# Optimization experiments

Hardware: AMD Instinct MI355X
Metric: run time of the kernel (lower is better)

Reference implementation:

```python
import jax, jax.numpy as jnp
import numpy as np

MARGIN = 0.2


def setup_inputs() -> dict:
    key = jax.random.key(0)
    k1, k2 = jax.random.split(key)
    N, D = 8192, 256
    im = jax.random.normal(k1, (N, D), dtype=jnp.float32)
    s = jax.random.normal(k2, (N, D), dtype=jnp.float32)
    return {"im": im, "s": s}


def reference(im, s):
    # scores[i, j] = <im_i, s_j>  (raw dot product, as in cosine_sim's mm)
    scores = im @ s.T                      # [N, N]
    diag = jnp.diagonal(scores)            # [N]

    # Rank of the diagonal element within each row / column of an ascending
    # sort == number of elements strictly smaller than it. This replaces the
    # original sort + host-side index search; weight = 1 / (rank + 1).
    # Ranks come from comparisons, so they carry no gradient (matching the
    # detached numpy computation in the original).
    rank1 = jnp.sum(scores < diag[:, None], axis=1)   # row rank of diag
    rank2 = jnp.sum(scores < diag[None, :], axis=0)   # col rank of diag
    w1 = 1.0 / (rank1.astype(scores.dtype) + 1.0)
    w2 = 1.0 / (rank2.astype(scores.dtype) + 1.0)

    # Hinge costs against the matched (diagonal) score.
    cost_s = jnp.maximum(MARGIN + scores - diag[:, None], 0.0)   # caption-retrieval
    cost_im = jnp.maximum(MARGIN + scores - diag[None, :], 0.0)  # image-retrieval

    # Zero out the diagonal (positive pairs).
    off_diag = ~jnp.eye(scores.shape[0], dtype=bool)
    cost_s = jnp.where(off_diag, cost_s, 0.0)
    cost_im = jnp.where(off_diag, cost_im, 0.0)

    # Hardest negative per row / column, rank-weighted.
    cost_s = w1 * jnp.max(cost_s, axis=1)
    cost_im = w2 * jnp.max(cost_im, axis=0)
    return jnp.sum(cost_s) + jnp.sum(cost_im)
```

## Files before the change

### kernel.cpp

```cpp
#include <hip/hip_runtime.h>
#include <stdint.h>

#define NROWS 8192
#define DDIM  256
#define K2    512
#define BLKSTRIDE 131072
#define MARGIN_F 0.2f
#define MFMA16 __builtin_amdgcn_mfma_f32_16x16x32_bf16
#define SBAR0() __builtin_amdgcn_sched_barrier(0)

typedef short  short8  __attribute__((ext_vector_type(8)));
typedef float  floatx4 __attribute__((ext_vector_type(4)));

__device__ unsigned short gA[(size_t)NROWS * K2];
__device__ unsigned short gB[(size_t)NROWS * K2];
__device__ float    g_diag[NROWS];
__device__ unsigned g_rowcnt[NROWS];
__device__ unsigned g_rowkey[NROWS];
__device__ unsigned g_colcnt[NROWS];
__device__ unsigned g_colkey[NROWS];

__device__ __forceinline__ unsigned short f2bf_rne(float x){
    unsigned u = __float_as_uint(x);
    return (unsigned short)((u + 0x7FFFu + ((u >> 16) & 1u)) >> 16);
}
__device__ __forceinline__ float bf2f(unsigned short h){
    return __uint_as_float(((unsigned)h) << 16);
}
__device__ __forceinline__ unsigned fkey(float f){
    unsigned u = __float_as_uint(f);
    return (u & 0x80000000u) ? ~u : (u | 0x80000000u);
}
__device__ __forceinline__ float kinv(unsigned k){
    unsigned u = (k & 0x80000000u) ? (k ^ 0x80000000u) : ~k;
    return __uint_as_float(u);
}
__device__ __forceinline__ unsigned bytesum(unsigned w){
    return (w & 0xFFu) + ((w >> 8) & 0xFFu) + ((w >> 16) & 0xFFu) + (w >> 24);
}

__device__ __forceinline__ void load_lds16(const unsigned short* gptr, void* lptr){
    __builtin_amdgcn_global_load_lds(
        (const __attribute__((address_space(1))) unsigned int*)(uintptr_t)gptr,
        (__attribute__((address_space(3))) unsigned int*)(unsigned)(uintptr_t)lptr,
        16, 0, 0);
}

__global__ __launch_bounds__(256) void prep_kernel(const float* __restrict__ im,
                                                   const float* __restrict__ s){
    const int w    = threadIdx.x >> 6;
    const int lane = threadIdx.x & 63;
    const int row  = blockIdx.x * 4 + w;

    const float4 a = ((const float4*)(im + (size_t)row * DDIM))[lane];
    const float4 b = ((const float4*)(s  + (size_t)row * DDIM))[lane];

    float dp = a.x*b.x + a.y*b.y + a.z*b.z + a.w*b.w;
    #pragma unroll
    for (int m = 1; m < 64; m <<= 1) dp += __shfl_xor(dp, m, 64);
    if (lane == 0){
        g_diag[row]   = dp;
        g_rowcnt[row] = 0u; g_rowkey[row] = 0u;
        g_colcnt[row] = 0u; g_colkey[row] = 0u;
    }

    float av[4] = {a.x, a.y, a.z, a.w};
    float bv[4] = {b.x, b.y, b.z, b.w};
    unsigned short ah[4], al[4], bh[4], bl[4];
    #pragma unroll
    for (int i = 0; i < 4; ++i){
        ah[i] = f2bf_rne(av[i]); al[i] = f2bf_rne(av[i] - bf2f(ah[i]));
        bh[i] = f2bf_rne(bv[i]); bl[i] = f2bf_rne(bv[i] - bf2f(bh[i]));
    }
    const int blk = row >> 8, r = row & 255;
    const int kc  = lane >> 3;
    const int sp  = (((lane & 7) >> 1) ^ ((r >> 1) & 3));
    const int hf  = (lane & 1) * 4;
    const size_t ub = (size_t)blk * BLKSTRIDE + (size_t)(kc * 2) * 8192
                    + (size_t)r * 32 + sp * 8 + hf;
    *(ushort4*)&gA[ub       ] = make_ushort4(ah[0], ah[1], ah[2], ah[3]);
    *(ushort4*)&gA[ub + 8192] = make_ushort4(al[0], al[1], al[2], al[3]);
    *(ushort4*)&gB[ub       ] = make_ushort4(bh[0], bh[1], bh[2], bh[3]);
    *(ushort4*)&gB[ub + 8192] = make_ushort4(bl[0], bl[1], bl[2], bl[3]);
}

__device__ __forceinline__ void stage_unit256(const unsigned short* __restrict__ Obase,
                                              int c, int hl, unsigned short* sb, int tid){
    const unsigned short* u = Obase + (size_t)(c * 2 + hl) * 8192;
    load_lds16(u + (size_t)tid * 8,        (char*)sb + tid * 16);
    load_lds16(u + 4096 + (size_t)tid * 8, (char*)sb + 8192 + tid * 16);
}

#define MFQ(A4, B4, MB) { \
    _Pragma("unroll") \
    for (int i_ = 0; i_ < 4; ++i_){ \
        _Pragma("unroll") \
        for (int nj_ = 0; nj_ < 4; ++nj_) \
            acc[(MB) + i_][nj_] = MFMA16((A4)[i_], (B4)[nj_], acc[(MB) + i_][nj_], 0, 0, 0); \
    } }
#define LDA4(U_, F_, MB) { \
    _Pragma("unroll") \
    for (int i_ = 0; i_ < 4; ++i_) \
        (F_)[i_] = *(const short8*)((const char*)(U_) + aoff + ((MB) + i_) * 1024); }
#define LDB4(U_, F_) { \
    _Pragma("unroll") \
    for (int nj_ = 0; nj_ < 4; ++nj_) \
        (F_)[nj_] = *(const short8*)((const char*)(U_) + boff + nj_ * 1024); }

__global__ __launch_bounds__(512, 2) void gemm_stats_kernel(){
    __shared__ unsigned short U[8][256 * 32];
    __shared__ float drow[256];
    __shared__ float dcol[256];

    const int tid = threadIdx.x;
    const int bid = blockIdx.x;
    const int bi  = (bid & 7) * 4 + ((bid >> 3) & 3);
    const int bj  = bid >> 5;

    if (tid < 256) drow[tid]       = g_diag[bi * 256 + tid];
    else           dcol[tid - 256] = g_diag[bj * 256 + (tid - 256)];

    const int w    = tid >> 6, lane = tid & 63;
    const int quad = lane >> 4, l16 = lane & 15;
    const int wr   = w >> 2,   wc  = w & 3;
    const int sel  = (quad ^ ((l16 >> 1) & 3)) << 4;
    const int aoff = (wr * 128 + l16) * 64 + sel;
    const int boff = (wc * 64  + l16) * 64 + sel;

    floatx4 acc[8][4] = {};

    const unsigned short* Abase = gA + (size_t)bi * BLKSTRIDE;
    const unsigned short* Bbase = gB + (size_t)bj * BLKSTRIDE;

    stage_unit256(Abase, 0, 0, U[0], tid);
    stage_unit256(Bbase, 0, 0, U[2], tid);
    stage_unit256(Abase, 0, 1, U[4], tid);
    stage_unit256(Bbase, 0, 1, U[6], tid);

    #pragma unroll 1
    for (int kc = 0; kc < 8; ++kc){
        const int d = kc & 1, e = d ^ 1;

        __builtin_amdgcn_s_barrier();
        SBAR0();
        if (kc < 7){
            stage_unit256(Abase, kc + 1, 0, U[0 + e], tid);
            stage_unit256(Bbase, kc + 1, 0, U[2 + e], tid);
            stage_unit256(Abase, kc + 1, 1, U[4 + e], tid);
            stage_unit256(Bbase, kc + 1, 1, U[6 + e], tid);
            SBAR0();
            asm volatile("s_waitcnt vmcnt(8)" ::: "memory");
        } else {
            asm volatile("s_waitcnt vmcnt(0)" ::: "memory");
        }
        __builtin_amdgcn_s_barrier();
        SBAR0();

        short8 ah[8], bh[4];
        LDA4(U[0 + d], &ah[0], 0); LDB4(U[2 + d], bh);
        __builtin_amdgcn_s_setprio(1); MFQ(&ah[0], bh, 0); __builtin_amdgcn_s_setprio(0);
        SBAR0();
        LDA4(U[0 + d], &ah[4], 4);
        __builtin_amdgcn_s_setprio(1); MFQ(&ah[4], bh, 4); __builtin_amdgcn_s_setprio(0);
        SBAR0();
        {
            short8 al0[4]; LDA4(U[4 + d], al0, 0);
            __builtin_amdgcn_s_setprio(1); MFQ(al0, bh, 0); __builtin_amdgcn_s_setprio(0);
            SBAR0();
        }
        {
            short8 al1[4]; LDA4(U[4 + d], al1, 4);
            __builtin_amdgcn_s_setprio(1); MFQ(al1, bh, 4); __builtin_amdgcn_s_setprio(0);
            SBAR0();
        }
        {
            short8 bl[4]; LDB4(U[6 + d], bl);
            __builtin_amdgcn_s_setprio(1); MFQ(&ah[0], bl, 0); __builtin_amdgcn_s_setprio(0);
            SBAR0();
            __builtin_amdgcn_s_setprio(1); MFQ(&ah[4], bl, 4); __builtin_amdgcn_s_setprio(0);
            SBAR0();
        }
    }

    __syncthreads();
    char* Lb = (char*)U;
    float*   RMX = (float*)Lb;
    uint8_t* RCN = (uint8_t*)(Lb + 69632);
    float*   CMX = (float*)(Lb + 88064);
    uint8_t* CCN = (uint8_t*)(Lb + 100352);

    const int c = wc * 16 + l16;
    const int q = wr * 4 + quad;

    #pragma unroll
    for (int mi = 0; mi < 8; ++mi){
        #pragma unroll
        for (int r = 0; r < 4; ++r){
            const int lrow = wr * 128 + mi * 16 + quad * 4 + r;
            const int gi   = bi * 256 + lrow;
            const float dv = drow[lrow];
            int cnt = 0; float mx = -3.0e38f;
            #pragma unroll
            for (int nj = 0; nj < 4; ++nj){
                const int gj  = bj * 256 + wc * 64 + nj * 16 + l16;
                const float v = acc[mi][nj][r];
                if (gi != gj){ cnt += (v < dv) ? 1 : 0; mx = fmaxf(mx, v); }
            }
            RMX[lrow * 68 + c] = mx;
            RCN[lrow * 72 + c] = (uint8_t)cnt;
        }
    }
    #pragma unroll
    for (int nj = 0; nj < 4; ++nj){
        const int lcol = wc * 64 + nj * 16 + l16;
        const int gj   = bj * 256 + lcol;
        const float dv = dcol[lcol];
        int cnt = 0; float mx = -3.0e38f;
        #pragma unroll
        for (int mi = 0; mi < 8; ++mi){
            #pragma unroll
            for (int r = 0; r < 4; ++r){
                const int gi  = bi * 256 + wr * 128 + mi * 16 + quad * 4 + r;
                const float v = acc[mi][nj][r];
                if (gi != gj){ cnt += (v < dv) ? 1 : 0; mx = fmaxf(mx, v); }
            }
        }
        CMX[lcol * 12 + q] = mx;
        CCN[lcol * 12 + q] = (uint8_t)cnt;
    }
    __syncthreads();

    if (tid < 256){
        const int lrow = tid, gi = bi * 256 + lrow;
        const float4* rp = (const float4*)(Lb + (size_t)lrow * 272);
        float mx = -3.0e38f;
        #pragma unroll
        for (int k = 0; k < 16; ++k){
            const float4 v = rp[k];
            mx = fmaxf(mx, fmaxf(fmaxf(v.x, v.y), fmaxf(v.z, v.w)));
        }
        const uint2* cp = (const uint2*)(Lb + 69632 + (size_t)lrow * 72);
        unsigned cs = 0;
        #pragma unroll
        for (int k = 0; k < 8; ++k){
            const uint2 wv = cp[k];
            cs += bytesum(wv.x) + bytesum(wv.y);
        }
        atomicAdd(&g_rowcnt[gi], cs);
        atomicMax(&g_rowkey[gi], fkey(mx));
    } else {
        const int lcol = tid - 256, gj = bj * 256 + lcol;
        const float4* qp = (const float4*)(Lb + 88064 + (size_t)lcol * 48);
        const float4 v0 = qp[0], v1 = qp[1];
        float mx = fmaxf(fmaxf(fmaxf(v0.x, v0.y), fmaxf(v0.z, v0.w)),
                         fmaxf(fmaxf(v1.x, v1.y), fmaxf(v1.z, v1.w)));
        const unsigned* cq = (const unsigned*)(Lb + 100352 + (size_t)lcol * 12);
        const unsigned cs = bytesum(cq[0]) + bytesum(cq[1]);
        atomicAdd(&g_colcnt[gj], cs);
        atomicMax(&g_colkey[gj], fkey(mx));
    }
}

__global__ __launch_bounds__(256) void finalize_kernel(float* __restrict__ out){
    __shared__ double red[256];
    double acc = 0.0;
    #pragma unroll
    for (int it = 0; it < NROWS / 256; ++it){
        const int i = it * 256 + threadIdx.x;
        const float d  = g_diag[i];
        const float cs  = fmaxf(MARGIN_F + kinv(g_rowkey[i]) - d, 0.0f) * (1.0f / (float)(g_rowcnt[i] + 1u));
        const float cim = fmaxf(MARGIN_F + kinv(g_colkey[i]) - d, 0.0f) * (1.0f / (float)(g_colcnt[i] + 1u));
        acc += (double)cs + (double)cim;
    }
    red[threadIdx.x] = acc;
    __syncthreads();
    for (int s2 = 128; s2 > 0; s2 >>= 1){
        if (threadIdx.x < s2) red[threadIdx.x] += red[threadIdx.x + s2];
        __syncthreads();
    }
    if (threadIdx.x == 0) out[0] = (float)red[0];
}

extern "C" void kernel_launch(void* const* d_in, const int* in_sizes, int n_in,
                              void* d_out, int out_size, void* d_ws, size_t ws_size,
                              hipStream_t stream){
    const float* im = (const float*)d_in[0];
    const float* s  = (const float*)d_in[1];
    float* out = (float*)d_out;

    prep_kernel<<<NROWS / 4, 256, 0, stream>>>(im, s);
    gemm_stats_kernel<<<1024, 512, 0, stream>>>();
    finalize_kernel<<<1, 256, 0, stream>>>(out);
}
```

Measured before the change: 171.0 us.

## Use 1024-thread GEMM blocks with 16 waves each owning 64x64 sub-tiles

The 256x256 GEMM tile goes from 8 waves (each computing 128x64) to 16 waves (each computing 64x64), so every wave keeps half as many accumulators. Staging now uses one 16-byte load per thread per unit, and the column-stats scratch layout and finalize kernel are widened to match the 16 waves. The aim is more waves to hide LDS and MFMA latency. In exchange, occupancy drops to one block per CU, each B and A fragment is reused less so LDS reads per MFMA go up, and the extra scheduling barriers are removed.

```diff
diff --git a/kernel.cpp b/kernel.cpp
--- a/kernel.cpp
+++ b/kernel.cpp
@@ -87,27 +87,22 @@
 __device__ __forceinline__ void stage_unit256(const unsigned short* __restrict__ Obase,
                                               int c, int hl, unsigned short* sb, int tid){
     const unsigned short* u = Obase + (size_t)(c * 2 + hl) * 8192;
-    load_lds16(u + (size_t)tid * 8,        (char*)sb + tid * 16);
-    load_lds16(u + 4096 + (size_t)tid * 8, (char*)sb + 8192 + tid * 16);
-}
-
-#define MFQ(A4, B4, MB) { \
+    load_lds16(u + (size_t)tid * 8, (char*)sb + tid * 16);
+}
+
+#define MFQ4(A4, B4) { \
     _Pragma("unroll") \
     for (int i_ = 0; i_ < 4; ++i_){ \
         _Pragma("unroll") \
         for (int nj_ = 0; nj_ < 4; ++nj_) \
-            acc[(MB) + i_][nj_] = MFMA16((A4)[i_], (B4)[nj_], acc[(MB) + i_][nj_], 0, 0, 0); \
+            acc[i_][nj_] = MFMA16((A4)[i_], (B4)[nj_], acc[i_][nj_], 0, 0, 0); \
     } }
-#define LDA4(U_, F_, MB) { \
+#define LD4(U_, F_, OFF_) { \
     _Pragma("unroll") \
     for (int i_ = 0; i_ < 4; ++i_) \
-        (F_)[i_] = *(const short8*)((const char*)(U_) + aoff + ((MB) + i_) * 1024); }
-#define LDB4(U_, F_) { \
-    _Pragma("unroll") \
-    for (int nj_ = 0; nj_ < 4; ++nj_) \
-        (F_)[nj_] = *(const short8*)((const char*)(U_) + boff + nj_ * 1024); }
-
-__global__ __launch_bounds__(512, 2) void gemm_stats_kernel(){
+        (F_)[i_] = *(const short8*)((const char*)(U_) + (OFF_) + i_ * 1024); }
+
+__global__ __launch_bounds__(1024, 1) void gemm_stats_kernel(){
     __shared__ unsigned short U[8][256 * 32];
     __shared__ float drow[256];
     __shared__ float dcol[256];
@@ -117,17 +112,17 @@
     const int bi  = (bid & 7) * 4 + ((bid >> 3) & 3);
     const int bj  = bid >> 5;
 
-    if (tid < 256) drow[tid]       = g_diag[bi * 256 + tid];
-    else           dcol[tid - 256] = g_diag[bj * 256 + (tid - 256)];
+    if (tid < 256)      drow[tid]       = g_diag[bi * 256 + tid];
+    else if (tid < 512) dcol[tid - 256] = g_diag[bj * 256 + (tid - 256)];
 
     const int w    = tid >> 6, lane = tid & 63;
     const int quad = lane >> 4, l16 = lane & 15;
     const int wr   = w >> 2,   wc  = w & 3;
     const int sel  = (quad ^ ((l16 >> 1) & 3)) << 4;
-    const int aoff = (wr * 128 + l16) * 64 + sel;
-    const int boff = (wc * 64  + l16) * 64 + sel;
-
-    floatx4 acc[8][4] = {};
+    const int aoff = (wr * 64 + l16) * 64 + sel;
+    const int boff = (wc * 64 + l16) * 64 + sel;
+
+    floatx4 acc[4][4] = {};
 
     const unsigned short* Abase = gA + (size_t)bi * BLKSTRIDE;
     const unsigned short* Bbase = gB + (size_t)bj * BLKSTRIDE;
@@ -149,36 +144,23 @@
             stage_unit256(Abase, kc + 1, 1, U[4 + e], tid);
             stage_unit256(Bbase, kc + 1, 1, U[6 + e], tid);
             SBAR0();
-            asm volatile("s_waitcnt vmcnt(8)" ::: "memory");
+            asm volatile("s_waitcnt vmcnt(4)" ::: "memory");
         } else {
             asm volatile("s_waitcnt vmcnt(0)" ::: "memory");
         }
         __builtin_amdgcn_s_barrier();
         SBAR0();
 
-        short8 ah[8], bh[4];
-        LDA4(U[0 + d], &ah[0], 0); LDB4(U[2 + d], bh);
-        __builtin_amdgcn_s_setprio(1); MFQ(&ah[0], bh, 0); __builtin_amdgcn_s_setprio(0);
-        SBAR0();
-        LDA4(U[0 + d], &ah[4], 4);
-        __builtin_amdgcn_s_setprio(1); MFQ(&ah[4], bh, 4); __builtin_amdgcn_s_setprio(0);
-        SBAR0();
+        short8 ah[4], bh[4];
+        LD4(U[0 + d], ah, aoff); LD4(U[2 + d], bh, boff);
+        __builtin_amdgcn_s_setprio(1); MFQ4(ah, bh); __builtin_amdgcn_s_setprio(0);
         {
-            short8 al0[4]; LDA4(U[4 + d], al0, 0);
-            __builtin_amdgcn_s_setprio(1); MFQ(al0, bh, 0); __builtin_amdgcn_s_setprio(0);
-            SBAR0();
+            short8 al[4]; LD4(U[4 + d], al, aoff);
+            __builtin_amdgcn_s_setprio(1); MFQ4(al, bh); __builtin_amdgcn_s_setprio(0);
         }
         {
-            short8 al1[4]; LDA4(U[4 + d], al1, 4);
-            __builtin_amdgcn_s_setprio(1); MFQ(al1, bh, 4); __builtin_amdgcn_s_setprio(0);
-            SBAR0();
-        }
-        {
-            short8 bl[4]; LDB4(U[6 + d], bl);
-            __builtin_amdgcn_s_setprio(1); MFQ(&ah[0], bl, 0); __builtin_amdgcn_s_setprio(0);
-            SBAR0();
-            __builtin_amdgcn_s_setprio(1); MFQ(&ah[4], bl, 4); __builtin_amdgcn_s_setprio(0);
-            SBAR0();
+            short8 bl[4]; LD4(U[6 + d], bl, boff);
+            __builtin_amdgcn_s_setprio(1); MFQ4(ah, bl); __builtin_amdgcn_s_setprio(0);
         }
     }
 
@@ -187,16 +169,16 @@
     float*   RMX = (float*)Lb;
     uint8_t* RCN = (uint8_t*)(Lb + 69632);
     float*   CMX = (float*)(Lb + 88064);
-    uint8_t* CCN = (uint8_t*)(Lb + 100352);
+    uint8_t* CCN = (uint8_t*)(Lb + 108544);
 
     const int c = wc * 16 + l16;
     const int q = wr * 4 + quad;
 
     #pragma unroll
-    for (int mi = 0; mi < 8; ++mi){
+    for (int mi = 0; mi < 4; ++mi){
         #pragma unroll
         for (int r = 0; r < 4; ++r){
-            const int lrow = wr * 128 + mi * 16 + quad * 4 + r;
+            const int lrow = wr * 64 + mi * 16 + quad * 4 + r;
             const int gi   = bi * 256 + lrow;
             const float dv = drow[lrow];
             int cnt = 0; float mx = -3.0e38f;
@@ -217,16 +199,16 @@
         const float dv = dcol[lcol];
         int cnt = 0; float mx = -3.0e38f;
         #pragma unroll
-        for (int mi = 0; mi < 8; ++mi){
+        for (int mi = 0; mi < 4; ++mi){
             #pragma unroll
             for (int r = 0; r < 4; ++r){
-                const int gi  = bi * 256 + wr * 128 + mi * 16 + quad * 4 + r;
+                const int gi  = bi * 256 + wr * 64 + mi * 16 + quad * 4 + r;
                 const float v = acc[mi][nj][r];
                 if (gi != gj){ cnt += (v < dv) ? 1 : 0; mx = fmaxf(mx, v); }
             }
         }
-        CMX[lcol * 12 + q] = mx;
-        CCN[lcol * 12 + q] = (uint8_t)cnt;
+        CMX[lcol * 20 + q] = mx;
+        CCN[lcol * 20 + q] = (uint8_t)cnt;
     }
     __syncthreads();
 
@@ -248,25 +230,30 @@
         }
         atomicAdd(&g_rowcnt[gi], cs);
         atomicMax(&g_rowkey[gi], fkey(mx));
-    } else {
+    } else if (tid < 512){
         const int lcol = tid - 256, gj = bj * 256 + lcol;
-        const float4* qp = (const float4*)(Lb + 88064 + (size_t)lcol * 48);
-        const float4 v0 = qp[0], v1 = qp[1];
-        float mx = fmaxf(fmaxf(fmaxf(v0.x, v0.y), fmaxf(v0.z, v0.w)),
-                         fmaxf(fmaxf(v1.x, v1.y), fmaxf(v1.z, v1.w)));
-        const unsigned* cq = (const unsigned*)(Lb + 100352 + (size_t)lcol * 12);
-        const unsigned cs = bytesum(cq[0]) + bytesum(cq[1]);
+        const float4* qp = (const float4*)(Lb + 88064 + (size_t)lcol * 80);
+        float mx = -3.0e38f;
+        #pragma unroll
+        for (int k = 0; k < 4; ++k){
+            const float4 v = qp[k];
+            mx = fmaxf(mx, fmaxf(fmaxf(v.x, v.y), fmaxf(v.z, v.w)));
+        }
+        const unsigned* cq = (const unsigned*)(Lb + 108544 + (size_t)lcol * 20);
+        unsigned cs = 0;
+        #pragma unroll
+        for (int k = 0; k < 4; ++k) cs += bytesum(cq[k]);
         atomicAdd(&g_colcnt[gj], cs);
         atomicMax(&g_colkey[gj], fkey(mx));
     }
 }
 
-__global__ __launch_bounds__(256) void finalize_kernel(float* __restrict__ out){
-    __shared__ double red[256];
+__global__ __launch_bounds__(1024) void finalize_kernel(float* __restrict__ out){
+    __shared__ double red[1024];
     double acc = 0.0;
     #pragma unroll
-    for (int it = 0; it < NROWS / 256; ++it){
-        const int i = it * 256 + threadIdx.x;
+    for (int it = 0; it < NROWS / 1024; ++it){
+        const int i = it * 1024 + threadIdx.x;
         const float d  = g_diag[i];
         const float cs  = fmaxf(MARGIN_F + kinv(g_rowkey[i]) - d, 0.0f) * (1.0f / (float)(g_rowcnt[i] + 1u));
         const float cim = fmaxf(MARGIN_F + kinv(g_colkey[i]) - d, 0.0f) * (1.0f / (float)(g_colcnt[i] + 1u));
@@ -274,7 +261,7 @@
     }
     red[threadIdx.x] = acc;
     __syncthreads();
-    for (int s2 = 128; s2 > 0; s2 >>= 1){
+    for (int s2 = 512; s2 > 0; s2 >>= 1){
         if (threadIdx.x < s2) red[threadIdx.x] += red[threadIdx.x + s2];
         __syncthreads();
     }
@@ -289,6 +276,6 @@
     float* out = (float*)d_out;
 
     prep_kernel<<<NROWS / 4, 256, 0, stream>>>(im, s);
-    gemm_stats_kernel<<<1024, 512, 0, stream>>>();
-    finalize_kernel<<<1, 256, 0, stream>>>(out);
-}
+    gemm_stats_kernel<<<1024, 1024, 0, stream>>>();
+    finalize_kernel<<<1, 1024, 0, stream>>>(out);
+}
```

New measurement: 163.9 us. 4.2% less time.
